# Performance work log

Measured on AMD Instinct MI355X. Metric: run time of the kernel, lower is better.

## Reference

```python
import jax, jax.numpy as jnp
import numpy as np

DIM = 1024
LATENT_DIM = 512
NUM_HEADS = 16
HEAD_DIM = DIM // NUM_HEADS
SCALE = HEAD_DIM ** -0.5


def setup_inputs() -> dict:
    key = jax.random.key(0)
    k1, k2, k3, k4, k5 = jax.random.split(key, 5)
    B, xN, zN = 2, 2048, 2048
    x = jax.random.normal(k1, (B, xN, DIM), dtype=jnp.float32)
    z = jax.random.normal(k2, (B, zN, LATENT_DIM), dtype=jnp.float32)
    # torch Linear weights: [out_features, in_features]
    Wq = jax.random.normal(k3, (DIM, DIM), dtype=jnp.float32) * (DIM ** -0.5)
    Wkv = jax.random.normal(k4, (2 * DIM, LATENT_DIM), dtype=jnp.float32) * (LATENT_DIM ** -0.5)
    Wo = jax.random.normal(k5, (DIM, DIM), dtype=jnp.float32) * (DIM ** -0.5)
    return {"x": x, "z": z, "Wq": Wq, "Wkv": Wkv, "Wo": Wo}


def reference(x, z, Wq, Wkv, Wo):
    B, xN, _ = x.shape
    _, zN, _ = z.shape
    # projections (torch Linear: y = x @ W.T)
    Q = (x @ Wq.T).reshape(B, xN, NUM_HEADS, HEAD_DIM)        # [B,xN,H,D]
    KV = (z @ Wkv.T).reshape(B, zN, 2, NUM_HEADS, HEAD_DIM)   # [B,zN,2,H,D]
    K = KV[:, :, 0]                                            # [B,zN,H,D]
    V = KV[:, :, 1]
    attn = jnp.einsum('bqhd,bkhd->bhqk', Q, K) * SCALE         # [B,H,xN,zN]
    attn = jax.nn.softmax(attn, axis=-1)
    O = jnp.einsum('bhqk,bkhd->bqhd', attn, V).reshape(B, xN, DIM)
    return O @ Wo.T
```

## Files before the change

### kernel.cpp

```cpp
#include <hip/hip_runtime.h>
#include <stdint.h>

#define SEQ 2048
#define QSCALE 0.1803368801111244f
#define DEFER_THR 11.5f

typedef __attribute__((ext_vector_type(8))) short bf16x8;
typedef __attribute__((ext_vector_type(4))) short bf16x4;
typedef __attribute__((ext_vector_type(4))) float f32x4;
typedef __attribute__((ext_vector_type(16))) float f32x16;
typedef unsigned short u16;

__device__ __forceinline__ u16 f2bf(float f) {
  union { float f; uint32_t u; } v; v.f = f;
  uint32_t u = v.u;
  u += 0x7fffu + ((u >> 16) & 1u);
  return (u16)(u >> 16);
}

__device__ __forceinline__ float fast_exp2(float x) {
#if __has_builtin(__builtin_amdgcn_exp2f)
  return __builtin_amdgcn_exp2f(x);
#else
  return exp2f(x);
#endif
}

__device__ __forceinline__ uint32_t cvtpk(float a, float b) {
  uint32_t r;
  asm("v_cvt_pk_bf16_f32 %0, %1, %2" : "=v"(r) : "v"(a), "v"(b));
  return r;
}

__device__ __forceinline__ void swap_pair(uint32_t& a, uint32_t& b, int hi) {
  uint32_t ta = (uint32_t)__shfl_xor((int)a, 32);
  uint32_t tb = (uint32_t)__shfl_xor((int)b, 32);
  a = hi ? tb : a;
  b = hi ? b : ta;
}

__device__ __forceinline__ void gload_lds16(const u16* g, u16* l) {
  __builtin_amdgcn_global_load_lds((__attribute__((address_space(1))) void*)g,
                                   (__attribute__((address_space(3))) void*)l,
                                   16, 0, 0);
}

__global__ void cvt5_kernel(const float* __restrict__ x, const float* __restrict__ z,
                            const float* __restrict__ Wq, const float* __restrict__ Wkv,
                            const float* __restrict__ Wo,
                            u16* __restrict__ xb, u16* __restrict__ zb,
                            u16* __restrict__ wqb, u16* __restrict__ wkvb,
                            u16* __restrict__ wob) {
  const int X4 = 1048576, Z4 = 524288, W4 = 262144;
  const int total = X4 + Z4 + 3 * W4;
  int i = blockIdx.x * blockDim.x + threadIdx.x;
  const int stride = gridDim.x * blockDim.x;
  for (; i < total; i += stride) {
    const float* src; u16* dst; int j = i;
    if (j < X4)              { src = x;   dst = xb; }
    else if ((j -= X4) < Z4) { src = z;   dst = zb; }
    else if ((j -= Z4) < W4) { src = Wq;  dst = wqb; }
    else if ((j -= W4) < W4) { src = Wkv; dst = wkvb; }
    else       { j -= W4;      src = Wo;  dst = wob; }
    float4 v = ((const float4*)src)[j];
    bf16x4 o;
    o[0] = (short)f2bf(v.x); o[1] = (short)f2bf(v.y);
    o[2] = (short)f2bf(v.z); o[3] = (short)f2bf(v.w);
    ((bf16x4*)dst)[j] = o;
  }
}

template <int BN, typename CT>
__device__ __forceinline__ void gemm_bt_body(const u16* __restrict__ A,
                                             const u16* __restrict__ B,
                                             CT* __restrict__ C,
                                             int N, int K, float scale,
                                             int tm, int tn, u16* As, u16* Bs) {
  constexpr int NB = BN / 32;
  constexpr int NBG = BN / 64;
  const int tid = threadIdx.x;
  const int wid = tid >> 6;
  const int lane = tid & 63;
  const int lg = lane >> 4, lq = lane & 15;
  const int wr = wid >> 1, wc = wid & 1;

  f32x4 acc[4][NB];
#pragma unroll
  for (int m = 0; m < 4; m++)
#pragma unroll
    for (int n = 0; n < NB; n++)
#pragma unroll
      for (int e = 0; e < 4; e++) acc[m][n][e] = 0.f;

  const int r0 = tid >> 2;
  const int s0 = tid & 3;
  const int sc = (s0 ^ ((r0 >> 1) & 3)) * 8;
  const u16* gA0 = A + (size_t)(tm * 128 + r0) * K + sc;
  const u16* gA1 = gA0 + (size_t)64 * K;
  const u16* gB0 = B + (size_t)(tn * BN + r0) * K + sc;
  const u16* gB1 = gB0 + (size_t)64 * K;
  u16* lA = As + wid * 512;
  u16* lB = Bs + wid * 512;

  const int rslot = (lg ^ ((lq >> 1) & 3)) * 8;

  for (int k0 = 0; k0 < K; k0 += 32) {
    __syncthreads();
    gload_lds16(gA0 + k0, lA);
    gload_lds16(gA1 + k0, lA + 2048);
    gload_lds16(gB0 + k0, lB);
    if constexpr (NBG == 2) gload_lds16(gB1 + k0, lB + 2048);
    __syncthreads();

    bf16x8 af[4], bfr[NB];
#pragma unroll
    for (int m = 0; m < 4; m++)
      af[m] = *(const bf16x8*)(As + (wr * 64 + m * 16 + lq) * 32 + rslot);
#pragma unroll
    for (int n = 0; n < NB; n++)
      bfr[n] = *(const bf16x8*)(Bs + (wc * (BN / 2) + n * 16 + lq) * 32 + rslot);
#pragma unroll
    for (int m = 0; m < 4; m++)
#pragma unroll
      for (int n = 0; n < NB; n++)
        acc[m][n] = __builtin_amdgcn_mfma_f32_16x16x32_bf16(af[m], bfr[n], acc[m][n], 0, 0, 0);
  }

#pragma unroll
  for (int m = 0; m < 4; m++) {
    const int row = tm * 128 + wr * 64 + m * 16 + lg * 4;
#pragma unroll
    for (int i = 0; i < 4; i++) {
      CT* cp = C + (size_t)(row + i) * N + tn * BN + wc * (BN / 2) + lq;
#pragma unroll
      for (int n = 0; n < NB; n++) {
        float v = acc[m][n][i] * scale;
        if constexpr (sizeof(CT) == 2) cp[n * 16] = (CT)f2bf(v);
        else                            cp[n * 16] = (CT)v;
      }
    }
  }
}

__global__ __launch_bounds__(256) void qkv_gemm(const u16* __restrict__ xb,
                                                const u16* __restrict__ zb,
                                                const u16* __restrict__ Wqb,
                                                const u16* __restrict__ Wkvb,
                                                u16* __restrict__ Qb,
                                                u16* __restrict__ Kb,
                                                u16* __restrict__ VTb) {
  __shared__ __align__(16) u16 As[128 * 32];
  __shared__ __align__(16) u16 Bs[128 * 32];
  int g = blockIdx.x;
  if (g < 256) {
    gemm_bt_body<128, u16>(xb, Wqb, Qb, 1024, 1024, QSCALE, g >> 3, g & 7, As, Bs);
  } else if (g < 512) {
    g -= 256;
    gemm_bt_body<128, u16>(zb, Wkvb, Kb, 1024, 512, 1.f, g >> 3, g & 7, As, Bs);
  } else {
    g -= 512;
    gemm_bt_body<128, u16>(Wkvb + 1024 * 512, zb, VTb, 4096, 512, 1.f, g >> 5, g & 31, As, Bs);
  }
}

__global__ __launch_bounds__(256) void o_gemm(const u16* __restrict__ Ob,
                                              const u16* __restrict__ Wob,
                                              float* __restrict__ out) {
  __shared__ __align__(16) u16 As[128 * 32];
  __shared__ __align__(16) u16 Bs[64 * 32];
  gemm_bt_body<64, float>(Ob, Wob, out, 1024, 1024, 1.f, blockIdx.y, blockIdx.x, As, Bs);
}

__global__ __launch_bounds__(256) void attn_kernel(const u16* __restrict__ Q,
                                                   const u16* __restrict__ K,
                                                   const u16* __restrict__ VT,
                                                   u16* __restrict__ O) {
  __shared__ __align__(16) u16 LDS[16384];

  const int tid = threadIdx.x;
  const int wid = tid >> 6;
  const int lane = tid & 63;
  const int l31 = lane & 31;
  const int hi = lane >> 5;

  const int bi = blockIdx.x;
  const int xcd = bi & 7, j = bi >> 3;
  const int qt = j & 15;
  const int bh = xcd + 8 * (j >> 4);
  const int b = bh >> 4, h = bh & 15;

  const int q0 = qt * 128 + wid * 32;

  bf16x8 qf[4];
  {
    const u16* qp = Q + (size_t)(b * SEQ + q0 + l31) * 1024 + h * 64 + hi * 8;
#pragma unroll
    for (int ks = 0; ks < 4; ks++) qf[ks] = *(const bf16x8*)(qp + ks * 16);
  }

  f32x16 of[2];
#pragma unroll
  for (int d = 0; d < 2; d++)
#pragma unroll
    for (int e = 0; e < 16; e++) of[d][e] = 0.f;
  float m_run = -3.0e38f, l_run = 0.f;

  const char* rdB[4];
#pragma unroll
  for (int ks = 0; ks < 4; ks++)
    rdB[ks] = (const char*)LDS + l31 * 128 + ((((2 * ks + hi) ^ (lane & 7))) << 4);

  const int r0 = tid >> 3;
  const int srcc = ((tid & 7) ^ (r0 & 7)) << 3;
  const u16* gK = K + (size_t)(b * SEQ + r0) * 1024 + h * 64 + srcc;
  const u16* gV = VT + (size_t)(h * 64 + r0) * 4096 + b * SEQ + srcc;
  u16* lK = LDS + wid * 512;
  u16* lV = LDS + 8192 + wid * 512;

  auto stage = [&](int t, int buf) {
    const u16* sk = gK + (size_t)t * 64 * 1024;
    gload_lds16(sk, lK + buf * 4096);
    gload_lds16(sk + (size_t)32 * 1024, lK + buf * 4096 + 2048);
    const u16* sv = gV + t * 64;
    gload_lds16(sv, lV + buf * 4096);
    gload_lds16(sv + (size_t)32 * 4096, lV + buf * 4096 + 2048);
  };

  auto tile_compute = [&](int buf) {
    const int bo = buf * 8192;

    f32x16 sacc[2];
#pragma unroll
    for (int kb = 0; kb < 2; kb++)
#pragma unroll
      for (int e = 0; e < 16; e++) sacc[kb][e] = 0.f;
    __builtin_amdgcn_s_setprio(1);
#pragma unroll
    for (int kb = 0; kb < 2; kb++)
#pragma unroll
      for (int ks = 0; ks < 4; ks++) {
        bf16x8 kf = *(const bf16x8*)(rdB[ks] + bo + kb * 4096);
        sacc[kb] = __builtin_amdgcn_mfma_f32_32x32x16_bf16(kf, qf[ks], sacc[kb], 0, 0, 0);
      }
    __builtin_amdgcn_s_setprio(0);

    float tmax = sacc[0][0];
#pragma unroll
    for (int e = 1; e < 16; e++) tmax = fmaxf(tmax, sacc[0][e]);
#pragma unroll
    for (int e = 0; e < 16; e++) tmax = fmaxf(tmax, sacc[1][e]);
    tmax = fmaxf(tmax, __shfl_xor(tmax, 32));

    if (!__all(tmax <= m_run + DEFER_THR)) {
      const float m_new = fmaxf(m_run, tmax);
      const float esc = fast_exp2(m_run - m_new);
      l_run *= esc;
#pragma unroll
      for (int r = 0; r < 16; r++) {
        const int qof = (r & 3) + 8 * (r >> 2) + 4 * hi;
        const float e = __shfl(esc, qof);
        of[0][r] *= e;
        of[1][r] *= e;
      }
      m_run = m_new;
    }

    float psum = 0.f;
#pragma unroll
    for (int kb = 0; kb < 2; kb++)
#pragma unroll
      for (int e = 0; e < 16; e++) {
        float p = fast_exp2(sacc[kb][e] - m_run);
        sacc[kb][e] = p;
        psum += p;
      }
    l_run += psum;

    bf16x8 pa[4];
#pragma unroll
    for (int kb = 0; kb < 2; kb++) {
      uint32_t c0 = cvtpk(sacc[kb][0],  sacc[kb][1]);
      uint32_t c1 = cvtpk(sacc[kb][2],  sacc[kb][3]);
      uint32_t c2 = cvtpk(sacc[kb][4],  sacc[kb][5]);
      uint32_t c3 = cvtpk(sacc[kb][6],  sacc[kb][7]);
      uint32_t c4 = cvtpk(sacc[kb][8],  sacc[kb][9]);
      uint32_t c5 = cvtpk(sacc[kb][10], sacc[kb][11]);
      uint32_t c6 = cvtpk(sacc[kb][12], sacc[kb][13]);
      uint32_t c7 = cvtpk(sacc[kb][14], sacc[kb][15]);
      swap_pair(c0, c2, hi);
      swap_pair(c1, c3, hi);
      swap_pair(c4, c6, hi);
      swap_pair(c5, c7, hi);
      union { bf16x8 v; uint32_t d[4]; } u0, u1;
      u0.d[0] = c0; u0.d[1] = c1; u0.d[2] = c2; u0.d[3] = c3;
      u1.d[0] = c4; u1.d[1] = c5; u1.d[2] = c6; u1.d[3] = c7;
      pa[2 * kb] = u0.v;
      pa[2 * kb + 1] = u1.v;
    }

    __builtin_amdgcn_s_setprio(1);
#pragma unroll
    for (int ks = 0; ks < 4; ks++)
#pragma unroll
      for (int db = 0; db < 2; db++) {
        bf16x8 vf = *(const bf16x8*)(rdB[ks] + bo + 16384 + db * 4096);
        of[db] = __builtin_amdgcn_mfma_f32_32x32x16_bf16(pa[ks], vf, of[db], 0, 0, 0);
      }
    __builtin_amdgcn_s_setprio(0);
  };

  stage(0, 0);
  __syncthreads();
  for (int kt = 0; kt < 32; kt += 2) {
    stage(kt + 1, 1);
    tile_compute(0);
    __syncthreads();
    if (kt + 2 < 32) stage(kt + 2, 0);
    tile_compute(1);
    __syncthreads();
  }

  const float lsum = l_run + __shfl_xor(l_run, 32);
  const float linv = 1.f / lsum;

#pragma unroll
  for (int r = 0; r < 16; r++) {
    const int qof = (r & 3) + 8 * (r >> 2) + 4 * hi;
    const float li = __shfl(linv, qof);
    u16* op = O + (size_t)(b * SEQ + q0 + qof) * 1024 + h * 64 + l31;
    op[0]  = f2bf(of[0][r] * li);
    op[32] = f2bf(of[1][r] * li);
  }
}

extern "C" void kernel_launch(void* const* d_in, const int* in_sizes, int n_in,
                              void* d_out, int out_size, void* d_ws, size_t ws_size,
                              hipStream_t stream) {
  const float* x   = (const float*)d_in[0];
  const float* z   = (const float*)d_in[1];
  const float* Wq  = (const float*)d_in[2];
  const float* Wkv = (const float*)d_in[3];
  const float* Wo  = (const float*)d_in[4];
  float* out = (float*)d_out;

  char* ws = (char*)d_ws;
  const size_t MB = 1024ull * 1024ull;
  u16* xb   = (u16*)(ws + 0);
  u16* zb   = (u16*)(ws + 8 * MB);
  u16* Wqb  = (u16*)(ws + 12 * MB);
  u16* Wkvb = (u16*)(ws + 14 * MB);
  u16* Wob  = (u16*)(ws + 16 * MB);
  u16* Qb   = (u16*)(ws + 18 * MB);
  u16* Kb   = (u16*)(ws + 26 * MB);
  u16* VTb  = (u16*)(ws + 34 * MB);
  u16* Ob   = (u16*)(ws + 42 * MB);

  cvt5_kernel<<<2048, 256, 0, stream>>>(x, z, Wq, Wkv, Wo, xb, zb, Wqb, Wkvb, Wob);

  qkv_gemm<<<768, 256, 0, stream>>>(xb, zb, Wqb, Wkvb, Qb, Kb, VTb);

  attn_kernel<<<512, 256, 0, stream>>>(Qb, Kb, VTb, Ob);

  o_gemm<<<dim3(16, 32), 256, 0, stream>>>(Ob, Wob, out);
}
```

Measured before the change: 117.3 us.

## Software-pipeline attention: overlap next tile's QK MFMA with current softmax and PV

Restructures the attention inner loop so K and V tiles are staged independently and the QK^T product for tile t+1 is issued before the softmax and PV of tile t. This lets the MFMA work of one tile hide the exp/max VALU work of the other. It also hoists the V fragment loads ahead of the softmax, splits the max and sum reductions into four independent chains, and adds a min-blocks-per-CU hint to launch bounds. In exchange it keeps two score accumulator sets live, which raises register pressure and may spill or reduce occupancy under the new launch bound.

```diff
diff --git a/kernel.cpp b/kernel.cpp
--- a/kernel.cpp
+++ b/kernel.cpp
@@ -171,10 +171,10 @@
   gemm_bt_body<64, float>(Ob, Wob, out, 1024, 1024, 1.f, blockIdx.y, blockIdx.x, As, Bs);
 }
 
-__global__ __launch_bounds__(256) void attn_kernel(const u16* __restrict__ Q,
-                                                   const u16* __restrict__ K,
-                                                   const u16* __restrict__ VT,
-                                                   u16* __restrict__ O) {
+__global__ __launch_bounds__(256, 2) void attn_kernel(const u16* __restrict__ Q,
+                                                      const u16* __restrict__ K,
+                                                      const u16* __restrict__ VT,
+                                                      u16* __restrict__ O) {
   __shared__ __align__(16) u16 LDS[16384];
 
   const int tid = threadIdx.x;
@@ -217,38 +217,53 @@
   u16* lK = LDS + wid * 512;
   u16* lV = LDS + 8192 + wid * 512;
 
-  auto stage = [&](int t, int buf) {
+  auto stageK = [&](int t, int par) {
     const u16* sk = gK + (size_t)t * 64 * 1024;
-    gload_lds16(sk, lK + buf * 4096);
-    gload_lds16(sk + (size_t)32 * 1024, lK + buf * 4096 + 2048);
+    gload_lds16(sk, lK + par * 4096);
+    gload_lds16(sk + (size_t)32 * 1024, lK + par * 4096 + 2048);
+  };
+  auto stageV = [&](int t, int par) {
     const u16* sv = gV + t * 64;
-    gload_lds16(sv, lV + buf * 4096);
-    gload_lds16(sv + (size_t)32 * 4096, lV + buf * 4096 + 2048);
+    gload_lds16(sv, lV + par * 4096);
+    gload_lds16(sv + (size_t)32 * 4096, lV + par * 4096 + 2048);
   };
 
-  auto tile_compute = [&](int buf) {
-    const int bo = buf * 8192;
-
-    f32x16 sacc[2];
+  auto qk = [&](f32x16 (&sn)[2], int kbyte) {
 #pragma unroll
     for (int kb = 0; kb < 2; kb++)
 #pragma unroll
-      for (int e = 0; e < 16; e++) sacc[kb][e] = 0.f;
+      for (int e = 0; e < 16; e++) sn[kb][e] = 0.f;
     __builtin_amdgcn_s_setprio(1);
 #pragma unroll
     for (int kb = 0; kb < 2; kb++)
 #pragma unroll
       for (int ks = 0; ks < 4; ks++) {
-        bf16x8 kf = *(const bf16x8*)(rdB[ks] + bo + kb * 4096);
-        sacc[kb] = __builtin_amdgcn_mfma_f32_32x32x16_bf16(kf, qf[ks], sacc[kb], 0, 0, 0);
+        bf16x8 kf = *(const bf16x8*)(rdB[ks] + kbyte + kb * 4096);
+        sn[kb] = __builtin_amdgcn_mfma_f32_32x32x16_bf16(kf, qf[ks], sn[kb], 0, 0, 0);
       }
     __builtin_amdgcn_s_setprio(0);
-
-    float tmax = sacc[0][0];
-#pragma unroll
-    for (int e = 1; e < 16; e++) tmax = fmaxf(tmax, sacc[0][e]);
-#pragma unroll
-    for (int e = 0; e < 16; e++) tmax = fmaxf(tmax, sacc[1][e]);
+  };
+
+  auto smpv = [&](f32x16 (&sc)[2], int vbyte) {
+    bf16x8 vf0[4], vf1[4];
+#pragma unroll
+    for (int ks = 0; ks < 4; ks++) {
+      vf0[ks] = *(const bf16x8*)(rdB[ks] + 16384 + vbyte);
+      vf1[ks] = *(const bf16x8*)(rdB[ks] + 16384 + vbyte + 4096);
+    }
+
+    float a0 = sc[0][0], a1 = sc[0][1], a2 = sc[0][2], a3 = sc[0][3];
+#pragma unroll
+    for (int e = 4; e < 16; e += 4) {
+      a0 = fmaxf(a0, sc[0][e]);     a1 = fmaxf(a1, sc[0][e + 1]);
+      a2 = fmaxf(a2, sc[0][e + 2]); a3 = fmaxf(a3, sc[0][e + 3]);
+    }
+#pragma unroll
+    for (int e = 0; e < 16; e += 4) {
+      a0 = fmaxf(a0, sc[1][e]);     a1 = fmaxf(a1, sc[1][e + 1]);
+      a2 = fmaxf(a2, sc[1][e + 2]); a3 = fmaxf(a3, sc[1][e + 3]);
+    }
+    float tmax = fmaxf(fmaxf(a0, a1), fmaxf(a2, a3));
     tmax = fmaxf(tmax, __shfl_xor(tmax, 32));
 
     if (!__all(tmax <= m_run + DEFER_THR)) {
@@ -265,28 +280,31 @@
       m_run = m_new;
     }
 
-    float psum = 0.f;
+    float s0 = 0.f, s1 = 0.f, s2 = 0.f, s3 = 0.f;
 #pragma unroll
     for (int kb = 0; kb < 2; kb++)
 #pragma unroll
-      for (int e = 0; e < 16; e++) {
-        float p = fast_exp2(sacc[kb][e] - m_run);
-        sacc[kb][e] = p;
-        psum += p;
+      for (int e = 0; e < 16; e += 4) {
+        float p0 = fast_exp2(sc[kb][e] - m_run);
+        float p1 = fast_exp2(sc[kb][e + 1] - m_run);
+        float p2 = fast_exp2(sc[kb][e + 2] - m_run);
+        float p3 = fast_exp2(sc[kb][e + 3] - m_run);
+        sc[kb][e] = p0; sc[kb][e + 1] = p1; sc[kb][e + 2] = p2; sc[kb][e + 3] = p3;
+        s0 += p0; s1 += p1; s2 += p2; s3 += p3;
       }
-    l_run += psum;
+    l_run += (s0 + s1) + (s2 + s3);
 
     bf16x8 pa[4];
 #pragma unroll
     for (int kb = 0; kb < 2; kb++) {
-      uint32_t c0 = cvtpk(sacc[kb][0],  sacc[kb][1]);
-      uint32_t c1 = cvtpk(sacc[kb][2],  sacc[kb][3]);
-      uint32_t c2 = cvtpk(sacc[kb][4],  sacc[kb][5]);
-      uint32_t c3 = cvtpk(sacc[kb][6],  sacc[kb][7]);
-      uint32_t c4 = cvtpk(sacc[kb][8],  sacc[kb][9]);
-      uint32_t c5 = cvtpk(sacc[kb][10], sacc[kb][11]);
-      uint32_t c6 = cvtpk(sacc[kb][12], sacc[kb][13]);
-      uint32_t c7 = cvtpk(sacc[kb][14], sacc[kb][15]);
+      uint32_t c0 = cvtpk(sc[kb][0],  sc[kb][1]);
+      uint32_t c1 = cvtpk(sc[kb][2],  sc[kb][3]);
+      uint32_t c2 = cvtpk(sc[kb][4],  sc[kb][5]);
+      uint32_t c3 = cvtpk(sc[kb][6],  sc[kb][7]);
+      uint32_t c4 = cvtpk(sc[kb][8],  sc[kb][9]);
+      uint32_t c5 = cvtpk(sc[kb][10], sc[kb][11]);
+      uint32_t c6 = cvtpk(sc[kb][12], sc[kb][13]);
+      uint32_t c7 = cvtpk(sc[kb][14], sc[kb][15]);
       swap_pair(c0, c2, hi);
       swap_pair(c1, c3, hi);
       swap_pair(c4, c6, hi);
@@ -300,25 +318,37 @@
 
     __builtin_amdgcn_s_setprio(1);
 #pragma unroll
-    for (int ks = 0; ks < 4; ks++)
-#pragma unroll
-      for (int db = 0; db < 2; db++) {
-        bf16x8 vf = *(const bf16x8*)(rdB[ks] + bo + 16384 + db * 4096);
-        of[db] = __builtin_amdgcn_mfma_f32_32x32x16_bf16(pa[ks], vf, of[db], 0, 0, 0);
-      }
+    for (int ks = 0; ks < 4; ks++) {
+      of[0] = __builtin_amdgcn_mfma_f32_32x32x16_bf16(pa[ks], vf0[ks], of[0], 0, 0, 0);
+      of[1] = __builtin_amdgcn_mfma_f32_32x32x16_bf16(pa[ks], vf1[ks], of[1], 0, 0, 0);
+    }
     __builtin_amdgcn_s_setprio(0);
   };
 
-  stage(0, 0);
+  f32x16 sA[2], sB[2];
+
+  stageK(0, 0); stageK(1, 1); stageV(0, 0);
   __syncthreads();
-  for (int kt = 0; kt < 32; kt += 2) {
-    stage(kt + 1, 1);
-    tile_compute(0);
+  qk(sA, 0);
+
+#pragma unroll 1
+  for (int t = 0; t < 30; t += 2) {
     __syncthreads();
-    if (kt + 2 < 32) stage(kt + 2, 0);
-    tile_compute(1);
+    stageK(t + 2, 0); stageV(t + 1, 1);
+    qk(sB, 8192);
+    smpv(sA, 0);
+
     __syncthreads();
-  }
+    stageK(t + 3, 1); stageV(t + 2, 0);
+    qk(sA, 0);
+    smpv(sB, 8192);
+  }
+  __syncthreads();
+  stageV(31, 1);
+  qk(sB, 8192);
+  smpv(sA, 0);
+  __syncthreads();
+  smpv(sB, 8192);
 
   const float lsum = l_run + __shfl_xor(l_run, 32);
   const float linv = 1.f / lsum;
```

Result: no change. 119.1 us (+1.5%).

## Split attention KV range in two with a combine kernel (flash-decoding style)

Applied to the files above, without the earlier changes.

Splits each attention block's 32 KV tiles into two halves, doubling the grid to 1024 blocks. Each half writes a normalized partial output plus its (max, sum) statistics, and a new combine kernel merges them into the final O. The goal is to raise occupancy and CU utilization, since 512 blocks underfill the device. It also adds launch_bounds occupancy 4 and breaks the max/sum reductions into four independent chains for ILP. In exchange it pays an extra kernel launch, the partial-output memory traffic, and a second bf16 rounding of the partials.

```diff
diff --git a/kernel.cpp b/kernel.cpp
--- a/kernel.cpp
+++ b/kernel.cpp
@@ -171,10 +171,11 @@
   gemm_bt_body<64, float>(Ob, Wob, out, 1024, 1024, 1.f, blockIdx.y, blockIdx.x, As, Bs);
 }
 
-__global__ __launch_bounds__(256) void attn_kernel(const u16* __restrict__ Q,
-                                                   const u16* __restrict__ K,
-                                                   const u16* __restrict__ VT,
-                                                   u16* __restrict__ O) {
+__global__ __launch_bounds__(256, 4) void attn_kernel(const u16* __restrict__ Q,
+                                                      const u16* __restrict__ K,
+                                                      const u16* __restrict__ VT,
+                                                      u16* __restrict__ OP,
+                                                      float2* __restrict__ ml) {
   __shared__ __align__(16) u16 LDS[16384];
 
   const int tid = threadIdx.x;
@@ -186,8 +187,10 @@
   const int bi = blockIdx.x;
   const int xcd = bi & 7, j = bi >> 3;
   const int qt = j & 15;
-  const int bh = xcd + 8 * (j >> 4);
+  const int s  = (j >> 4) & 1;
+  const int bh = xcd + 8 * (j >> 5);
   const int b = bh >> 4, h = bh & 15;
+  const int t0 = s * 16;
 
   const int q0 = qt * 128 + wid * 32;
 
@@ -244,11 +247,18 @@
       }
     __builtin_amdgcn_s_setprio(0);
 
-    float tmax = sacc[0][0];
-#pragma unroll
-    for (int e = 1; e < 16; e++) tmax = fmaxf(tmax, sacc[0][e]);
-#pragma unroll
-    for (int e = 0; e < 16; e++) tmax = fmaxf(tmax, sacc[1][e]);
+    float a0 = sacc[0][0], a1 = sacc[0][1], a2 = sacc[0][2], a3 = sacc[0][3];
+#pragma unroll
+    for (int e = 4; e < 16; e += 4) {
+      a0 = fmaxf(a0, sacc[0][e]);     a1 = fmaxf(a1, sacc[0][e + 1]);
+      a2 = fmaxf(a2, sacc[0][e + 2]); a3 = fmaxf(a3, sacc[0][e + 3]);
+    }
+#pragma unroll
+    for (int e = 0; e < 16; e += 4) {
+      a0 = fmaxf(a0, sacc[1][e]);     a1 = fmaxf(a1, sacc[1][e + 1]);
+      a2 = fmaxf(a2, sacc[1][e + 2]); a3 = fmaxf(a3, sacc[1][e + 3]);
+    }
+    float tmax = fmaxf(fmaxf(a0, a1), fmaxf(a2, a3));
     tmax = fmaxf(tmax, __shfl_xor(tmax, 32));
 
     if (!__all(tmax <= m_run + DEFER_THR)) {
@@ -265,16 +275,19 @@
       m_run = m_new;
     }
 
-    float psum = 0.f;
+    float s0 = 0.f, s1 = 0.f, s2 = 0.f, s3 = 0.f;
 #pragma unroll
     for (int kb = 0; kb < 2; kb++)
 #pragma unroll
-      for (int e = 0; e < 16; e++) {
-        float p = fast_exp2(sacc[kb][e] - m_run);
-        sacc[kb][e] = p;
-        psum += p;
+      for (int e = 0; e < 16; e += 4) {
+        float p0 = fast_exp2(sacc[kb][e] - m_run);
+        float p1 = fast_exp2(sacc[kb][e + 1] - m_run);
+        float p2 = fast_exp2(sacc[kb][e + 2] - m_run);
+        float p3 = fast_exp2(sacc[kb][e + 3] - m_run);
+        sacc[kb][e] = p0; sacc[kb][e + 1] = p1; sacc[kb][e + 2] = p2; sacc[kb][e + 3] = p3;
+        s0 += p0; s1 += p1; s2 += p2; s3 += p3;
       }
-    l_run += psum;
+    l_run += (s0 + s1) + (s2 + s3);
 
     bf16x8 pa[4];
 #pragma unroll
@@ -309,13 +322,14 @@
     __builtin_amdgcn_s_setprio(0);
   };
 
-  stage(0, 0);
+  stage(t0, 0);
   __syncthreads();
-  for (int kt = 0; kt < 32; kt += 2) {
-    stage(kt + 1, 1);
+#pragma unroll 1
+  for (int tt = 0; tt < 16; tt += 2) {
+    stage(t0 + tt + 1, 1);
     tile_compute(0);
     __syncthreads();
-    if (kt + 2 < 32) stage(kt + 2, 0);
+    if (tt < 14) stage(t0 + tt + 2, 0);
     tile_compute(1);
     __syncthreads();
   }
@@ -323,14 +337,45 @@
   const float lsum = l_run + __shfl_xor(l_run, 32);
   const float linv = 1.f / lsum;
 
+  u16* OPs = OP + (size_t)s * 4096 * 1024;
 #pragma unroll
   for (int r = 0; r < 16; r++) {
     const int qof = (r & 3) + 8 * (r >> 2) + 4 * hi;
     const float li = __shfl(linv, qof);
-    u16* op = O + (size_t)(b * SEQ + q0 + qof) * 1024 + h * 64 + l31;
+    u16* op = OPs + (size_t)(b * SEQ + q0 + qof) * 1024 + h * 64 + l31;
     op[0]  = f2bf(of[0][r] * li);
     op[32] = f2bf(of[1][r] * li);
   }
+  if (hi == 0) {
+    const int grow = b * SEQ + q0 + l31;
+    ml[s * (4096 * 16) + grow * 16 + h] = make_float2(m_run, lsum);
+  }
+}
+
+__global__ __launch_bounds__(256) void combine_kernel(const u16* __restrict__ OP,
+                                                      const float2* __restrict__ ml,
+                                                      u16* __restrict__ Ob) {
+  const int i = blockIdx.x * 256 + threadIdx.x;
+  const int grow = i >> 7;
+  const int h = (i >> 3) & 15;
+  const float2 a0 = ml[grow * 16 + h];
+  const float2 a1 = ml[4096 * 16 + grow * 16 + h];
+  const float M = fmaxf(a0.x, a1.x);
+  float w0 = a0.y * fast_exp2(a0.x - M);
+  float w1 = a1.y * fast_exp2(a1.x - M);
+  const float inv = 1.f / (w0 + w1);
+  w0 *= inv; w1 *= inv;
+  const bf16x8 p0 = ((const bf16x8*)OP)[i];
+  const bf16x8 p1 = ((const bf16x8*)(OP + (size_t)4096 * 1024))[i];
+  bf16x8 o;
+#pragma unroll
+  for (int e = 0; e < 8; e++) {
+    union { uint32_t u; float f; } f0, f1;
+    f0.u = ((uint32_t)(u16)p0[e]) << 16;
+    f1.u = ((uint32_t)(u16)p1[e]) << 16;
+    o[e] = (short)f2bf(w0 * f0.f + w1 * f1.f);
+  }
+  ((bf16x8*)Ob)[i] = o;
 }
 
 extern "C" void kernel_launch(void* const* d_in, const int* in_sizes, int n_in,
@@ -354,12 +399,16 @@
   u16* Kb   = (u16*)(ws + 26 * MB);
   u16* VTb  = (u16*)(ws + 34 * MB);
   u16* Ob   = (u16*)(ws + 42 * MB);
+  u16* OP   = (u16*)(ws + 0);
+  float2* ml = (float2*)(ws + 50 * MB);
 
   cvt5_kernel<<<2048, 256, 0, stream>>>(x, z, Wq, Wkv, Wo, xb, zb, Wqb, Wkvb, Wob);
 
   qkv_gemm<<<768, 256, 0, stream>>>(xb, zb, Wqb, Wkvb, Qb, Kb, VTb);
 
-  attn_kernel<<<512, 256, 0, stream>>>(Qb, Kb, VTb, Ob);
+  attn_kernel<<<1024, 256, 0, stream>>>(Qb, Kb, VTb, OP, ml);
+
+  combine_kernel<<<2048, 256, 0, stream>>>(OP, ml, Ob);
 
   o_gemm<<<dim3(16, 32), 256, 0, stream>>>(Ob, Wob, out);
 }
```

After: 121.8 us. +3.8%, slower.
